# Kernel optimization log

Hardware: AMD Instinct MI355X
Metric: run time of the kernel (lower is better)

## Reference

```python
import jax, jax.numpy as jnp
import numpy as np
import math

D_MODEL = 1024
N_HEADS = 16
D_HEAD = D_MODEL // N_HEADS
B, S = 4, 2048


def setup_inputs() -> dict:
    key = jax.random.key(0)
    ks = jax.random.split(key, 9)
    std = 1.0 / math.sqrt(D_MODEL)
    x = jax.random.normal(ks[0], (B, S, D_MODEL), dtype=jnp.float32)
    # causal mask: True = masked out
    mask = jnp.triu(jnp.ones((S, S), dtype=bool), k=1)
    Wq = jax.random.normal(ks[1], (D_MODEL, D_MODEL), jnp.float32) * std
    bq = jnp.zeros((D_MODEL,), jnp.float32)
    Wk = jax.random.normal(ks[2], (D_MODEL, D_MODEL), jnp.float32) * std
    bk = jnp.zeros((D_MODEL,), jnp.float32)
    Wv = jax.random.normal(ks[3], (D_MODEL, D_MODEL), jnp.float32) * std
    bv = jnp.zeros((D_MODEL,), jnp.float32)
    Wo = jax.random.normal(ks[4], (D_MODEL, D_MODEL), jnp.float32) * std
    bo = jnp.zeros((D_MODEL,), jnp.float32)
    return {"x": x, "mask": mask, "Wq": Wq, "bq": bq, "Wk": Wk, "bk": bk,
            "Wv": Wv, "bv": bv, "Wo": Wo, "bo": bo}


def reference(x, mask, Wq, bq, Wk, bk, Wv, bv, Wo, bo):
    b, s, _ = x.shape
    scale = math.sqrt(D_HEAD)
    # projections (Linear: x @ W.T + b), reshape to [b, h, s, d]
    def proj(W, bias):
        y = jnp.einsum('bsd,ed->bse', x, W) + bias
        return y.reshape(b, s, N_HEADS, D_HEAD).transpose(0, 2, 1, 3)
    q = proj(Wq, bq)
    k = proj(Wk, bk)
    v = proj(Wv, bv)
    scores = jnp.einsum('bhqd,bhkd->bhqk', q, k) / scale  # [b,h,s,s]
    scores = jnp.where(mask[None, None, :, :], -jnp.inf, scores)
    attn = jax.nn.softmax(scores, axis=-1)
    # dropout is identity in eval mode
    out = jnp.einsum('bhqk,bhkd->bhqd', attn, v)
    out = out.transpose(0, 2, 1, 3).reshape(b, s, D_MODEL)
    return jnp.einsum('bsd,ed->bse', out, Wo) + bo
```

## Files before the change

kernel.cpp:

```cpp
#include <hip/hip_runtime.h>
#include <stdint.h>

#define NH 16
#define DH 64
#define DM 1024
#define Bz 4
#define Sz 2048

typedef __bf16 bf16x8 __attribute__((ext_vector_type(8)));
typedef float f32x4 __attribute__((ext_vector_type(4)));

#define GLD_LDS16(gsrc, ldst)                                             \
    __builtin_amdgcn_global_load_lds(                                     \
        (const __attribute__((address_space(1))) void*)(gsrc),            \
        (__attribute__((address_space(3))) void*)(ldst), 16, 0, 0)

__device__ __forceinline__ unsigned short f2bf(float f) {
    unsigned u = __float_as_uint(f);
    u += 0x7FFFu + ((u >> 16) & 1u);
    return (unsigned short)(u >> 16);
}
__device__ __forceinline__ float bf2f(unsigned short h) {
    return __uint_as_float(((unsigned)h) << 16);
}

__global__ void detect_dtype(const unsigned short* __restrict__ xs,
                             int* __restrict__ flagp)
{
    const int t = threadIdx.x;
    int cnt = 0;
    for (int i = 0; i < 64; i++) {
        const unsigned short h = xs[(t * 64 + i) * 2];
        const int e = (h >> 7) & 0xFF;
        if (h != 0 && e >= 100 && e <= 130) cnt++;
    }
#pragma unroll
    for (int off = 32; off >= 1; off >>= 1)
        cnt += __shfl_xor(cnt, off);
    if (t == 0) *flagp = (cnt < 2048) ? 1 : 0;
}

__global__ __launch_bounds__(256) void convert_inputs(
    const void* s0, const void* s1, const void* s2, const void* s3,
    const void* s4, const void* s5, const void* s6, const void* s7,
    const void* s8,
    unsigned short* d0, unsigned short* d1, unsigned short* d2,
    unsigned short* d3, unsigned short* d4, unsigned short* d5,
    unsigned short* d6, unsigned short* d7, unsigned short* d8,
    const int* __restrict__ flagp)
{
    const void* s; unsigned short* d; int n;
    switch (blockIdx.y) {
        case 0: s = s0; d = d0; n = Bz * Sz * DM; break;
        case 1: s = s1; d = d1; n = DM * DM; break;
        case 2: s = s2; d = d2; n = DM * DM; break;
        case 3: s = s3; d = d3; n = DM * DM; break;
        case 4: s = s4; d = d4; n = DM * DM; break;
        case 5: s = s5; d = d5; n = DM; break;
        case 6: s = s6; d = d6; n = DM; break;
        case 7: s = s7; d = d7; n = DM; break;
        default: s = s8; d = d8; n = DM; break;
    }
    const int flag   = *flagp;
    const int stride = gridDim.x * blockDim.x * 4;
    const int base   = (blockIdx.x * blockDim.x + threadIdx.x) * 4;
    if (flag) {
        const float* sf = (const float*)s;
        for (int i = base; i < n; i += stride) {
            const float4 v = *reinterpret_cast<const float4*>(&sf[i]);
            ushort2 a, b;
            a.x = f2bf(v.x); a.y = f2bf(v.y);
            b.x = f2bf(v.z); b.y = f2bf(v.w);
            *reinterpret_cast<ushort2*>(&d[i])     = a;
            *reinterpret_cast<ushort2*>(&d[i + 2]) = b;
        }
    } else {
        const unsigned short* sh = (const unsigned short*)s;
        for (int i = base; i < n; i += stride)
            *reinterpret_cast<uint2*>(&d[i]) = *reinterpret_cast<const uint2*>(&sh[i]);
    }
}

__global__ __launch_bounds__(256) void gemm_qkv(
    const unsigned short* __restrict__ X,
    const unsigned short* __restrict__ Wq,
    const unsigned short* __restrict__ Wk,
    const unsigned short* __restrict__ Wv,
    const unsigned short* __restrict__ bq,
    const unsigned short* __restrict__ bk,
    const unsigned short* __restrict__ bv,
    unsigned short* __restrict__ Qb,
    unsigned short* __restrict__ Kb,
    unsigned short* __restrict__ Vtb)
{
    __shared__ __align__(16) unsigned short As[4][128 * 32];
    __shared__ __align__(16) unsigned short Bs[4][128 * 32];
    const int tid  = threadIdx.x;
    const int w    = tid >> 6, lane = tid & 63;
    const int quad = lane >> 4, l15 = lane & 15;
    const int wm   = (w & 1) * 64, wn = (w >> 1) * 64;

    const int flat = (int)(blockIdx.y * gridDim.x + blockIdx.x);
    const int k8   = flat & 7;
    const int m    = flat >> 3;
    const int proj = m >> 6;
    const int mm   = m & 63;
    const int bm   = (k8 * 8 + (mm >> 3)) * 128;
    const int bn   = (mm & 7) * 128;

    const unsigned short* W      = proj == 0 ? Wq : (proj == 1 ? Wk : Wv);
    const unsigned short* bias_p = proj == 0 ? bq : (proj == 1 ? bk : bv);

    const int lrow = lane >> 2;
    const int lcol = (lane & 3) * 8;

    f32x4 acc[4][4];
    for (int i = 0; i < 4; i++)
        for (int j = 0; j < 4; j++)
            acc[i][j] = f32x4{0.f, 0.f, 0.f, 0.f};

    auto stage = [&](int buf, int ks) {
        const int k0 = ks << 5;
#pragma unroll
        for (int t = 0; t < 2; t++) {
            const int r = w * 32 + t * 16;
            GLD_LDS16(&X[(size_t)(bm + r + lrow) * DM + k0 + lcol], &As[buf][r * 32]);
            GLD_LDS16(&W[(size_t)(bn + r + lrow) * DM + k0 + lcol], &Bs[buf][r * 32]);
        }
    };

    auto compute32 = [&](int cur) {
        bf16x8 af[4], bfr[4];
#pragma unroll
        for (int i = 0; i < 4; i++)
            af[i] = *reinterpret_cast<const bf16x8*>(&As[cur][(wm + i * 16 + l15) * 32 + quad * 8]);
#pragma unroll
        for (int j = 0; j < 4; j++)
            bfr[j] = *reinterpret_cast<const bf16x8*>(&Bs[cur][(wn + j * 16 + l15) * 32 + quad * 8]);
#pragma unroll
        for (int i = 0; i < 4; i++)
#pragma unroll
            for (int j = 0; j < 4; j++)
                acc[i][j] = __builtin_amdgcn_mfma_f32_16x16x32_bf16(af[i], bfr[j], acc[i][j], 0, 0, 0);
    };

    stage(0, 0);
    stage(1, 1);
    for (int t = 0; t < 30; ++t) {
        stage((t + 2) & 3, t + 2);
        asm volatile("s_waitcnt vmcnt(8)" ::: "memory");
        __builtin_amdgcn_s_barrier();
        compute32(t & 3);
    }
    asm volatile("s_waitcnt vmcnt(4)" ::: "memory");
    __builtin_amdgcn_s_barrier();
    compute32(30 & 3);
    asm volatile("s_waitcnt vmcnt(0)" ::: "memory");
    __builtin_amdgcn_s_barrier();
    compute32(31 & 3);

    if (proj < 2) {
        unsigned short* dst = (proj == 0) ? Qb : Kb;
#pragma unroll
        for (int j = 0; j < 4; j++) {
            const int   e    = bn + wn + j * 16 + l15;
            const int   h    = e >> 6, dd = e & 63;
            const float bias = bf2f(bias_p[e]);
#pragma unroll
            for (int i = 0; i < 4; i++) {
#pragma unroll
                for (int r = 0; r < 4; r++) {
                    const int mrow = bm + wm + i * 16 + quad * 4 + r;
                    const int b = mrow >> 11, s = mrow & 2047;
                    dst[((size_t)(b * NH + h) * Sz + s) * DH + dd] = f2bf(acc[i][j][r] + bias);
                }
            }
        }
    } else {
#pragma unroll
        for (int j = 0; j < 4; j++) {
            const int   e    = bn + wn + j * 16 + l15;
            const int   h    = e >> 6, dd = e & 63;
            const float bias = bf2f(bias_p[e]);
#pragma unroll
            for (int i = 0; i < 4; i++) {
                const int m0 = bm + wm + i * 16 + quad * 4;
                const int b  = m0 >> 11, s0 = m0 & 2047;
                const unsigned u0 = __float_as_uint(acc[i][j][0] + bias) + 0x8000u;
                const unsigned u1 = __float_as_uint(acc[i][j][1] + bias) + 0x8000u;
                const unsigned u2 = __float_as_uint(acc[i][j][2] + bias) + 0x8000u;
                const unsigned u3 = __float_as_uint(acc[i][j][3] + bias) + 0x8000u;
                uint2 pk;
                pk.x = __builtin_amdgcn_perm(u1, u0, 0x07060302u);
                pk.y = __builtin_amdgcn_perm(u3, u2, 0x07060302u);
                *reinterpret_cast<uint2*>(
                    &Vtb[((size_t)(b * NH + h) * DH + dd) * Sz + s0]) = pk;
            }
        }
    }
}

__global__ __launch_bounds__(512) void flash_attn(
    const unsigned short* __restrict__ Qb,
    const unsigned short* __restrict__ Kb,
    const unsigned short* __restrict__ Vtb,
    unsigned short* __restrict__ AOb)
{
    __shared__ __align__(16) unsigned short Ks[64 * 72];
    __shared__ __align__(16) unsigned short Vs[64 * 72];
    __shared__ __align__(16) unsigned short Ps[128 * 72];

    const int tid  = threadIdx.x;
    const int w    = tid >> 6, lane = tid & 63;
    const int quad = lane >> 4, l15 = lane & 15;

    const int flat = (int)(blockIdx.y * gridDim.x + blockIdx.x);
    const int k8   = flat & 7;
    const int m    = flat >> 3;
    const int bh   = k8 + 8 * (m >> 3);
    const int cA   = m & 7;

    const int srow = tid >> 3;
    const int scc  = (tid & 7) * 8;
    const int hh = bh & 15, bb = bh >> 4;

    for (int pass = 0; pass < 2; pass++) {
        const int chunk = pass ? (15 - cA) : cA;
        const int qb = chunk * 128;
        const int qw = qb + w * 16;

        const size_t qbase = ((size_t)bh * Sz + qw + l15) * DH;
        const bf16x8 qf0 = *reinterpret_cast<const bf16x8*>(&Qb[qbase + quad * 8]);
        const bf16x8 qf1 = *reinterpret_cast<const bf16x8*>(&Qb[qbase + 32 + quad * 8]);

        f32x4 o[4];
#pragma unroll
        for (int jd = 0; jd < 4; jd++) o[jd] = f32x4{0.f, 0.f, 0.f, 0.f};
        float lsum = 0.f;

        const int n_kv = qb + 128;

        auto compute = [&](int kb) {
            const bool need_mask = (kb + 64 > qw);
#pragma unroll
            for (int j = 0; j < 4; j++) {
                const bf16x8 kf0 = *reinterpret_cast<const bf16x8*>(&Ks[(j * 16 + l15) * 72 + quad * 8]);
                const bf16x8 kf1 = *reinterpret_cast<const bf16x8*>(&Ks[(j * 16 + l15) * 72 + 32 + quad * 8]);
                f32x4 st = f32x4{0.f, 0.f, 0.f, 0.f};
                st = __builtin_amdgcn_mfma_f32_16x16x32_bf16(kf0, qf0, st, 0, 0, 0);
                st = __builtin_amdgcn_mfma_f32_16x16x32_bf16(kf1, qf1, st, 0, 0, 0);
                const int qa = qw + l15;
                float p[4];
#pragma unroll
                for (int r = 0; r < 4; r++) {
                    float e = __builtin_amdgcn_exp2f(st[r] * 0.18033688011f);
                    if (need_mask) {
                        const int kv = kb + j * 16 + quad * 4 + r;
                        e = (kv <= qa) ? e : 0.f;
                    }
                    p[r] = e;
                }
                lsum += (p[0] + p[1]) + (p[2] + p[3]);
                const unsigned u0 = __float_as_uint(p[0]) + 0x8000u;
                const unsigned u1 = __float_as_uint(p[1]) + 0x8000u;
                const unsigned u2 = __float_as_uint(p[2]) + 0x8000u;
                const unsigned u3 = __float_as_uint(p[3]) + 0x8000u;
                const unsigned pk0 = __builtin_amdgcn_perm(u1, u0, 0x07060302u);
                const unsigned pk1 = __builtin_amdgcn_perm(u3, u2, 0x07060302u);
                const int prow = (w * 16 + l15) * 72 + j * 16 + quad * 4;
                *reinterpret_cast<unsigned*>(&Ps[prow])     = pk0;
                *reinterpret_cast<unsigned*>(&Ps[prow + 2]) = pk1;
            }

            asm volatile("s_waitcnt lgkmcnt(0)" ::: "memory");

            const bf16x8 pf0 = *reinterpret_cast<const bf16x8*>(&Ps[(w * 16 + l15) * 72 + quad * 8]);
            const bf16x8 pf1 = *reinterpret_cast<const bf16x8*>(&Ps[(w * 16 + l15) * 72 + 32 + quad * 8]);
#pragma unroll
            for (int jd = 0; jd < 4; jd++) {
                const bf16x8 vf0 = *reinterpret_cast<const bf16x8*>(&Vs[(jd * 16 + l15) * 72 + quad * 8]);
                const bf16x8 vf1 = *reinterpret_cast<const bf16x8*>(&Vs[(jd * 16 + l15) * 72 + 32 + quad * 8]);
                o[jd] = __builtin_amdgcn_mfma_f32_16x16x32_bf16(pf0, vf0, o[jd], 0, 0, 0);
                o[jd] = __builtin_amdgcn_mfma_f32_16x16x32_bf16(pf1, vf1, o[jd], 0, 0, 0);
            }
        };

        uint4 kr0 = *reinterpret_cast<const uint4*>(&Kb[((size_t)bh * Sz + srow) * DH + scc]);
        uint4 vr0 = *reinterpret_cast<const uint4*>(&Vtb[((size_t)bh * DH + srow) * Sz + scc]);
        uint4 kr1, vr1;

        for (int kb = 0; kb < n_kv; kb += 128) {
            __syncthreads();
            *reinterpret_cast<uint4*>(&Ks[srow * 72 + scc]) = kr0;
            *reinterpret_cast<uint4*>(&Vs[srow * 72 + scc]) = vr0;
            kr1 = *reinterpret_cast<const uint4*>(&Kb[((size_t)bh * Sz + kb + 64 + srow) * DH + scc]);
            vr1 = *reinterpret_cast<const uint4*>(&Vtb[((size_t)bh * DH + srow) * Sz + kb + 64 + scc]);
            asm volatile("s_waitcnt lgkmcnt(0)" ::: "memory");
            __builtin_amdgcn_s_barrier();
            asm volatile("" ::: "memory");
            if (kb <= qw + 15) compute(kb);

            __syncthreads();
            *reinterpret_cast<uint4*>(&Ks[srow * 72 + scc]) = kr1;
            *reinterpret_cast<uint4*>(&Vs[srow * 72 + scc]) = vr1;
            if (kb + 128 < n_kv) {
                kr0 = *reinterpret_cast<const uint4*>(&Kb[((size_t)bh * Sz + kb + 128 + srow) * DH + scc]);
                vr0 = *reinterpret_cast<const uint4*>(&Vtb[((size_t)bh * DH + srow) * Sz + kb + 128 + scc]);
            }
            asm volatile("s_waitcnt lgkmcnt(0)" ::: "memory");
            __builtin_amdgcn_s_barrier();
            asm volatile("" ::: "memory");
            if (kb + 64 <= qw + 15) compute(kb + 64);
        }

        lsum += __shfl_xor(lsum, 16);
        lsum += __shfl_xor(lsum, 32);

        float linv[4];
#pragma unroll
        for (int r = 0; r < 4; r++)
            linv[r] = 1.0f / __shfl(lsum, quad * 4 + r);
#pragma unroll
        for (int jd = 0; jd < 4; jd++) {
#pragma unroll
            for (int r = 0; r < 4; r++) {
                const int s = qw + quad * 4 + r;
                AOb[((size_t)(bb * Sz + s)) * DM + hh * DH + jd * 16 + l15] =
                    f2bf(o[jd][r] * linv[r]);
            }
        }
    }
}

__global__ __launch_bounds__(256) void gemm_out(
    const unsigned short* __restrict__ A,
    const unsigned short* __restrict__ W,
    const unsigned short* __restrict__ bo,
    void* __restrict__ outv,
    const int* __restrict__ flagp)
{
    __shared__ __align__(16) unsigned short As[4][128 * 32];
    __shared__ __align__(16) unsigned short Bs[4][128 * 32];
    const int tid  = threadIdx.x;
    const int w    = tid >> 6, lane = tid & 63;
    const int quad = lane >> 4, l15 = lane & 15;
    const int wm   = (w & 1) * 64, wn = (w >> 1) * 64;

    const int flat = (int)(blockIdx.y * gridDim.x + blockIdx.x);
    const int k8   = flat & 7;
    const int m    = flat >> 3;
    const int bm   = (k8 * 8 + (m >> 3)) * 128;
    const int bn   = (m & 7) * 128;

    const int lrow = lane >> 2;
    const int lcol = (lane & 3) * 8;

    f32x4 acc[4][4];
    for (int i = 0; i < 4; i++)
        for (int j = 0; j < 4; j++)
            acc[i][j] = f32x4{0.f, 0.f, 0.f, 0.f};

    auto stage = [&](int buf, int ks) {
        const int k0 = ks << 5;
#pragma unroll
        for (int t = 0; t < 2; t++) {
            const int r = w * 32 + t * 16;
            GLD_LDS16(&A[(size_t)(bm + r + lrow) * DM + k0 + lcol], &As[buf][r * 32]);
            GLD_LDS16(&W[(size_t)(bn + r + lrow) * DM + k0 + lcol], &Bs[buf][r * 32]);
        }
    };

    auto compute32 = [&](int cur) {
        bf16x8 af[4], bfr[4];
#pragma unroll
        for (int i = 0; i < 4; i++)
            af[i] = *reinterpret_cast<const bf16x8*>(&As[cur][(wm + i * 16 + l15) * 32 + quad * 8]);
#pragma unroll
        for (int j = 0; j < 4; j++)
            bfr[j] = *reinterpret_cast<const bf16x8*>(&Bs[cur][(wn + j * 16 + l15) * 32 + quad * 8]);
#pragma unroll
        for (int i = 0; i < 4; i++)
#pragma unroll
            for (int j = 0; j < 4; j++)
                acc[i][j] = __builtin_amdgcn_mfma_f32_16x16x32_bf16(af[i], bfr[j], acc[i][j], 0, 0, 0);
    };

    stage(0, 0);
    stage(1, 1);
    for (int t = 0; t < 30; ++t) {
        stage((t + 2) & 3, t + 2);
        asm volatile("s_waitcnt vmcnt(8)" ::: "memory");
        __builtin_amdgcn_s_barrier();
        compute32(t & 3);
    }
    asm volatile("s_waitcnt vmcnt(4)" ::: "memory");
    __builtin_amdgcn_s_barrier();
    compute32(30 & 3);
    asm volatile("s_waitcnt vmcnt(0)" ::: "memory");
    __builtin_amdgcn_s_barrier();
    compute32(31 & 3);

    const int flag = *flagp;
    float*          outf = (float*)outv;
    unsigned short* outh = (unsigned short*)outv;
#pragma unroll
    for (int j = 0; j < 4; j++) {
        const int   e    = bn + wn + j * 16 + l15;
        const float bias = bf2f(bo[e]);
#pragma unroll
        for (int i = 0; i < 4; i++) {
#pragma unroll
            for (int r = 0; r < 4; r++) {
                const int   mrow = bm + wm + i * 16 + quad * 4 + r;
                const float v = acc[i][j][r] + bias;
                if (flag) outf[(size_t)mrow * DM + e] = v;
                else      outh[(size_t)mrow * DM + e] = f2bf(v);
            }
        }
    }
}

extern "C" void kernel_launch(void* const* d_in, const int* in_sizes, int n_in,
                              void* d_out, int out_size, void* d_ws, size_t ws_size,
                              hipStream_t stream) {
    const void* x = nullptr;
    const void* Wsrc[4] = {nullptr, nullptr, nullptr, nullptr};
    const void* bsrc[4] = {nullptr, nullptr, nullptr, nullptr};
    int nw = 0, nb = 0;
    for (int i = 0; i < n_in; i++) {
        const int sz = in_sizes[i];
        if (sz == Bz * Sz * DM)            { if (!x) x = d_in[i]; }
        else if (sz == DM * DM)            { if (nw < 4) Wsrc[nw++] = d_in[i]; }
        else if (sz == DM)                 { if (nb < 4) bsrc[nb++] = d_in[i]; }
    }

    char* wsb = (char*)d_ws;
    int*  flagp = (int*)wsb;
    unsigned short* Xc  = (unsigned short*)(wsb + 16);
    const size_t NX = (size_t)Bz * Sz * DM;
    const size_t NW = (size_t)DM * DM;
    unsigned short* Wc0 = Xc  + NX;
    unsigned short* Wc1 = Wc0 + NW;
    unsigned short* Wc2 = Wc1 + NW;
    unsigned short* Wc3 = Wc2 + NW;
    unsigned short* bc0 = Wc3 + NW;
    unsigned short* bc1 = bc0 + DM;
    unsigned short* bc2 = bc1 + DM;
    unsigned short* bc3 = bc2 + DM;
    unsigned short* Qb  = bc3 + DM;
    const size_t SZ = (size_t)Bz * NH * Sz * DH;
    unsigned short* Kb  = Qb  + SZ;
    unsigned short* Vtb = Kb  + SZ;
    unsigned short* AOb = Vtb + SZ;

    detect_dtype<<<1, 64, 0, stream>>>((const unsigned short*)x, flagp);
    convert_inputs<<<dim3(512, 9), 256, 0, stream>>>(
        x, Wsrc[0], Wsrc[1], Wsrc[2], Wsrc[3],
        bsrc[0], bsrc[1], bsrc[2], bsrc[3],
        Xc, Wc0, Wc1, Wc2, Wc3, bc0, bc1, bc2, bc3, flagp);

    gemm_qkv <<<dim3(24, 64), 256, 0, stream>>>(Xc, Wc0, Wc1, Wc2, bc0, bc1, bc2, Qb, Kb, Vtb);
    flash_attn<<<dim3(8, 64), 512, 0, stream>>>(Qb, Kb, Vtb, AOb);
    gemm_out <<<dim3(8, 64), 256, 0, stream>>>(AOb, Wc3, bc3, d_out, flagp);
}
```

Before: 303.6 us.

## Retile QKV and output GEMMs to 256x256 blocks with swizzled LDS

Both projection GEMMs move from 128x128 tiles with a 4-stage K=32 pipeline to 256x256 tiles using 512 threads, K=64 double-buffered LDS staging, and an XOR-swizzled LDS layout. MFMA groups are wrapped in s_setprio. The intent is more data reuse per block, fewer LDS bank conflicts, and better overlap of math with global loads. The cost is a large LDS footprint of 128KB per block, which limits how many blocks fit per CU. Grids also shrink to 384 and 128 blocks, so the output GEMM may leave many CUs idle and the work may be spread unevenly.

Result: slower. 316.4 us (+4.2%).

```diff
diff --git a/kernel.cpp b/kernel.cpp
--- a/kernel.cpp
+++ b/kernel.cpp
@@ -6,6 +6,7 @@
 #define DM 1024
 #define Bz 4
 #define Sz 2048
+#define NKT 16
 
 typedef __bf16 bf16x8 __attribute__((ext_vector_type(8)));
 typedef float f32x4 __attribute__((ext_vector_type(4)));
@@ -81,7 +82,14 @@
     }
 }
 
-__global__ __launch_bounds__(256) void gemm_qkv(
+
+__device__ __forceinline__ bf16x8 lds_frag(const unsigned short* lds, int R, int c) {
+    const int cs = c ^ ((R & 7) << 4);
+    return *reinterpret_cast<const bf16x8*>(
+        reinterpret_cast<const char*>(lds) + R * 128 + cs);
+}
+
+__global__ __launch_bounds__(512, 2) void gemm_qkv(
     const unsigned short* __restrict__ X,
     const unsigned short* __restrict__ Wq,
     const unsigned short* __restrict__ Wk,
@@ -93,103 +101,157 @@
     unsigned short* __restrict__ Kb,
     unsigned short* __restrict__ Vtb)
 {
-    __shared__ __align__(16) unsigned short As[4][128 * 32];
-    __shared__ __align__(16) unsigned short Bs[4][128 * 32];
+    __shared__ __align__(16) unsigned short Alds[2][256 * 64];
+    __shared__ __align__(16) unsigned short Blds[2][256 * 64];
+
     const int tid  = threadIdx.x;
     const int w    = tid >> 6, lane = tid & 63;
     const int quad = lane >> 4, l15 = lane & 15;
-    const int wm   = (w & 1) * 64, wn = (w >> 1) * 64;
-
-    const int flat = (int)(blockIdx.y * gridDim.x + blockIdx.x);
+    const int wr   = w >> 2, wc = w & 3;
+
+    const int flat = (int)blockIdx.x;
     const int k8   = flat & 7;
     const int m    = flat >> 3;
-    const int proj = m >> 6;
-    const int mm   = m & 63;
-    const int bm   = (k8 * 8 + (mm >> 3)) * 128;
-    const int bn   = (mm & 7) * 128;
+    const int proj = m >> 4;
+    const int mm   = m & 15;
+    const int bm   = (k8 * 4 + (mm >> 2)) * 256;
+    const int bn   = (mm & 3) * 256;
 
     const unsigned short* W      = proj == 0 ? Wq : (proj == 1 ? Wk : Wv);
     const unsigned short* bias_p = proj == 0 ? bq : (proj == 1 ? bk : bv);
-
-    const int lrow = lane >> 2;
-    const int lcol = (lane & 3) * 8;
-
-    f32x4 acc[4][4];
-    for (int i = 0; i < 4; i++)
+    const unsigned short* Abase  = X + (size_t)bm * DM;
+    const unsigned short* Bbase  = W + (size_t)bn * DM;
+
+    const int srow = 8 * w + (lane >> 3);
+    const int scb  = (lane & 7) * 16;
+    const int ssc  = scb ^ ((srow & 7) << 4);
+
+    f32x4 acc[8][4];
+#pragma unroll
+    for (int i = 0; i < 8; i++)
+#pragma unroll
         for (int j = 0; j < 4; j++)
             acc[i][j] = f32x4{0.f, 0.f, 0.f, 0.f};
 
-    auto stage = [&](int buf, int ks) {
-        const int k0 = ks << 5;
-#pragma unroll
-        for (int t = 0; t < 2; t++) {
-            const int r = w * 32 + t * 16;
-            GLD_LDS16(&X[(size_t)(bm + r + lrow) * DM + k0 + lcol], &As[buf][r * 32]);
-            GLD_LDS16(&W[(size_t)(bn + r + lrow) * DM + k0 + lcol], &Bs[buf][r * 32]);
+    auto stage_tile = [&](int buf, int kt) {
+        const int kc = kt * 64;
+#pragma unroll
+        for (int q = 0; q < 2; q++) {
+            const int r  = srow + 64 * q;
+            const int ld = (64 * q + 8 * w) * 64;
+            GLD_LDS16(&Abase[(size_t)(r      ) * DM + kc + (ssc >> 1)], &Alds[buf][ld]);
+            GLD_LDS16(&Abase[(size_t)(r + 128) * DM + kc + (ssc >> 1)], &Alds[buf][ld + 128 * 64]);
+            GLD_LDS16(&Bbase[(size_t)(r      ) * DM + kc + (ssc >> 1)], &Blds[buf][ld]);
+            GLD_LDS16(&Bbase[(size_t)(r + 128) * DM + kc + (ssc >> 1)], &Blds[buf][ld + 128 * 64]);
         }
     };
 
-    auto compute32 = [&](int cur) {
-        bf16x8 af[4], bfr[4];
-#pragma unroll
-        for (int i = 0; i < 4; i++)
-            af[i] = *reinterpret_cast<const bf16x8*>(&As[cur][(wm + i * 16 + l15) * 32 + quad * 8]);
-#pragma unroll
-        for (int j = 0; j < 4; j++)
-            bfr[j] = *reinterpret_cast<const bf16x8*>(&Bs[cur][(wn + j * 16 + l15) * 32 + quad * 8]);
-#pragma unroll
-        for (int i = 0; i < 4; i++)
-#pragma unroll
-            for (int j = 0; j < 4; j++)
-                acc[i][j] = __builtin_amdgcn_mfma_f32_16x16x32_bf16(af[i], bfr[j], acc[i][j], 0, 0, 0);
-    };
-
-    stage(0, 0);
-    stage(1, 1);
-    for (int t = 0; t < 30; ++t) {
-        stage((t + 2) & 3, t + 2);
-        asm volatile("s_waitcnt vmcnt(8)" ::: "memory");
-        __builtin_amdgcn_s_barrier();
-        compute32(t & 3);
-    }
-    asm volatile("s_waitcnt vmcnt(4)" ::: "memory");
-    __builtin_amdgcn_s_barrier();
-    compute32(30 & 3);
+    stage_tile(0, 0);
     asm volatile("s_waitcnt vmcnt(0)" ::: "memory");
     __builtin_amdgcn_s_barrier();
-    compute32(31 & 3);
+    asm volatile("" ::: "memory");
+
+    for (int T = 0; T < NKT; ++T) {
+        const int cur = T & 1;
+        if (T < NKT - 1) stage_tile(cur ^ 1, T + 1);
+
+        const unsigned short* A = &Alds[cur][0];
+        const unsigned short* B = &Blds[cur][0];
+        const int aR0 = wr * 128 + l15;
+        const int bR0 = wc * 64 + l15;
+
+        bf16x8 aR[4][2], b01[2][2], b23[2][2];
+#pragma unroll
+        for (int mi = 0; mi < 4; mi++) {
+            aR[mi][0] = lds_frag(A, aR0 + mi * 16, quad * 16);
+            aR[mi][1] = lds_frag(A, aR0 + mi * 16, quad * 16 + 64);
+        }
+#pragma unroll
+        for (int nj = 0; nj < 2; nj++) {
+            b01[nj][0] = lds_frag(B, bR0 + nj * 16, quad * 16);
+            b01[nj][1] = lds_frag(B, bR0 + nj * 16, quad * 16 + 64);
+        }
+        __builtin_amdgcn_s_setprio(1);
+#pragma unroll
+        for (int mi = 0; mi < 4; mi++)
+#pragma unroll
+            for (int nj = 0; nj < 2; nj++) {
+                acc[mi][nj] = __builtin_amdgcn_mfma_f32_16x16x32_bf16(aR[mi][0], b01[nj][0], acc[mi][nj], 0, 0, 0);
+                acc[mi][nj] = __builtin_amdgcn_mfma_f32_16x16x32_bf16(aR[mi][1], b01[nj][1], acc[mi][nj], 0, 0, 0);
+            }
+        __builtin_amdgcn_s_setprio(0);
+#pragma unroll
+        for (int nj = 0; nj < 2; nj++) {
+            b23[nj][0] = lds_frag(B, bR0 + (nj + 2) * 16, quad * 16);
+            b23[nj][1] = lds_frag(B, bR0 + (nj + 2) * 16, quad * 16 + 64);
+        }
+        __builtin_amdgcn_s_setprio(1);
+#pragma unroll
+        for (int mi = 0; mi < 4; mi++)
+#pragma unroll
+            for (int nj = 0; nj < 2; nj++) {
+                acc[mi][nj + 2] = __builtin_amdgcn_mfma_f32_16x16x32_bf16(aR[mi][0], b23[nj][0], acc[mi][nj + 2], 0, 0, 0);
+                acc[mi][nj + 2] = __builtin_amdgcn_mfma_f32_16x16x32_bf16(aR[mi][1], b23[nj][1], acc[mi][nj + 2], 0, 0, 0);
+            }
+        __builtin_amdgcn_s_setprio(0);
+#pragma unroll
+        for (int mi = 0; mi < 4; mi++) {
+            aR[mi][0] = lds_frag(A, aR0 + (mi + 4) * 16, quad * 16);
+            aR[mi][1] = lds_frag(A, aR0 + (mi + 4) * 16, quad * 16 + 64);
+        }
+        __builtin_amdgcn_s_setprio(1);
+#pragma unroll
+        for (int mi = 0; mi < 4; mi++)
+#pragma unroll
+            for (int nj = 0; nj < 2; nj++) {
+                acc[mi + 4][nj + 2] = __builtin_amdgcn_mfma_f32_16x16x32_bf16(aR[mi][0], b23[nj][0], acc[mi + 4][nj + 2], 0, 0, 0);
+                acc[mi + 4][nj + 2] = __builtin_amdgcn_mfma_f32_16x16x32_bf16(aR[mi][1], b23[nj][1], acc[mi + 4][nj + 2], 0, 0, 0);
+            }
+#pragma unroll
+        for (int mi = 0; mi < 4; mi++)
+#pragma unroll
+            for (int nj = 0; nj < 2; nj++) {
+                acc[mi + 4][nj] = __builtin_amdgcn_mfma_f32_16x16x32_bf16(aR[mi][0], b01[nj][0], acc[mi + 4][nj], 0, 0, 0);
+                acc[mi + 4][nj] = __builtin_amdgcn_mfma_f32_16x16x32_bf16(aR[mi][1], b01[nj][1], acc[mi + 4][nj], 0, 0, 0);
+            }
+        __builtin_amdgcn_s_setprio(0);
+
+        asm volatile("s_waitcnt vmcnt(0)" ::: "memory");
+        __builtin_amdgcn_s_barrier();
+        asm volatile("" ::: "memory");
+    }
 
     if (proj < 2) {
         unsigned short* dst = (proj == 0) ? Qb : Kb;
 #pragma unroll
-        for (int j = 0; j < 4; j++) {
-            const int   e    = bn + wn + j * 16 + l15;
+        for (int nj = 0; nj < 4; nj++) {
+            const int   e    = bn + wc * 64 + nj * 16 + l15;
             const int   h    = e >> 6, dd = e & 63;
             const float bias = bf2f(bias_p[e]);
 #pragma unroll
-            for (int i = 0; i < 4; i++) {
+            for (int mi = 0; mi < 8; mi++) {
 #pragma unroll
                 for (int r = 0; r < 4; r++) {
-                    const int mrow = bm + wm + i * 16 + quad * 4 + r;
+                    const int mrow = bm + wr * 128 + mi * 16 + quad * 4 + r;
                     const int b = mrow >> 11, s = mrow & 2047;
-                    dst[((size_t)(b * NH + h) * Sz + s) * DH + dd] = f2bf(acc[i][j][r] + bias);
+                    dst[((size_t)(b * NH + h) * Sz + s) * DH + dd] = f2bf(acc[mi][nj][r] + bias);
                 }
             }
         }
     } else {
 #pragma unroll
-        for (int j = 0; j < 4; j++) {
-            const int   e    = bn + wn + j * 16 + l15;
+        for (int nj = 0; nj < 4; nj++) {
+            const int   e    = bn + wc * 64 + nj * 16 + l15;
             const int   h    = e >> 6, dd = e & 63;
             const float bias = bf2f(bias_p[e]);
 #pragma unroll
-            for (int i = 0; i < 4; i++) {
-                const int m0 = bm + wm + i * 16 + quad * 4;
+            for (int mi = 0; mi < 8; mi++) {
+                const int m0 = bm + wr * 128 + mi * 16 + quad * 4;
                 const int b  = m0 >> 11, s0 = m0 & 2047;
-                const unsigned u0 = __float_as_uint(acc[i][j][0] + bias) + 0x8000u;
-                const unsigned u1 = __float_as_uint(acc[i][j][1] + bias) + 0x8000u;
-                const unsigned u2 = __float_as_uint(acc[i][j][2] + bias) + 0x8000u;
-                const unsigned u3 = __float_as_uint(acc[i][j][3] + bias) + 0x8000u;
+                const unsigned u0 = __float_as_uint(acc[mi][nj][0] + bias) + 0x8000u;
+                const unsigned u1 = __float_as_uint(acc[mi][nj][1] + bias) + 0x8000u;
+                const unsigned u2 = __float_as_uint(acc[mi][nj][2] + bias) + 0x8000u;
+                const unsigned u3 = __float_as_uint(acc[mi][nj][3] + bias) + 0x8000u;
                 uint2 pk;
                 pk.x = __builtin_amdgcn_perm(u1, u0, 0x07060302u);
                 pk.y = __builtin_amdgcn_perm(u3, u2, 0x07060302u);
@@ -332,87 +394,142 @@
     }
 }
 
-__global__ __launch_bounds__(256) void gemm_out(
-    const unsigned short* __restrict__ A,
+__global__ __launch_bounds__(512, 2) void gemm_out(
+    const unsigned short* __restrict__ Ain,
     const unsigned short* __restrict__ W,
     const unsigned short* __restrict__ bo,
     void* __restrict__ outv,
     const int* __restrict__ flagp)
 {
-    __shared__ __align__(16) unsigned short As[4][128 * 32];
-    __shared__ __align__(16) unsigned short Bs[4][128 * 32];
+    __shared__ __align__(16) unsigned short Alds[2][256 * 64];
+    __shared__ __align__(16) unsigned short Blds[2][256 * 64];
+
     const int tid  = threadIdx.x;
     const int w    = tid >> 6, lane = tid & 63;
     const int quad = lane >> 4, l15 = lane & 15;
-    const int wm   = (w & 1) * 64, wn = (w >> 1) * 64;
-
-    const int flat = (int)(blockIdx.y * gridDim.x + blockIdx.x);
+    const int wr   = w >> 2, wc = w & 3;
+
+    const int flat = (int)blockIdx.x;
     const int k8   = flat & 7;
     const int m    = flat >> 3;
-    const int bm   = (k8 * 8 + (m >> 3)) * 128;
-    const int bn   = (m & 7) * 128;
-
-    const int lrow = lane >> 2;
-    const int lcol = (lane & 3) * 8;
-
-    f32x4 acc[4][4];
-    for (int i = 0; i < 4; i++)
+    const int bm   = (k8 * 4 + (m >> 2)) * 256;
+    const int bn   = (m & 3) * 256;
+
+    const unsigned short* Abase = Ain + (size_t)bm * DM;
+    const unsigned short* Bbase = W   + (size_t)bn * DM;
+
+    const int srow = 8 * w + (lane >> 3);
+    const int scb  = (lane & 7) * 16;
+    const int ssc  = scb ^ ((srow & 7) << 4);
+
+    f32x4 acc[8][4];
+#pragma unroll
+    for (int i = 0; i < 8; i++)
+#pragma unroll
         for (int j = 0; j < 4; j++)
             acc[i][j] = f32x4{0.f, 0.f, 0.f, 0.f};
 
-    auto stage = [&](int buf, int ks) {
-        const int k0 = ks << 5;
-#pragma unroll
-        for (int t = 0; t < 2; t++) {
-            const int r = w * 32 + t * 16;
-            GLD_LDS16(&A[(size_t)(bm + r + lrow) * DM + k0 + lcol], &As[buf][r * 32]);
-            GLD_LDS16(&W[(size_t)(bn + r + lrow) * DM + k0 + lcol], &Bs[buf][r * 32]);
+    auto stage_tile = [&](int buf, int kt) {
+        const int kc = kt * 64;
+#pragma unroll
+        for (int q = 0; q < 2; q++) {
+            const int r  = srow + 64 * q;
+            const int ld = (64 * q + 8 * w) * 64;
+            GLD_LDS16(&Abase[(size_t)(r      ) * DM + kc + (ssc >> 1)], &Alds[buf][ld]);
+            GLD_LDS16(&Abase[(size_t)(r + 128) * DM + kc + (ssc >> 1)], &Alds[buf][ld + 128 * 64]);
+            GLD_LDS16(&Bbase[(size_t)(r      ) * DM + kc + (ssc >> 1)], &Blds[buf][ld]);
+            GLD_LDS16(&Bbase[(size_t)(r + 128) * DM + kc + (ssc >> 1)], &Blds[buf][ld + 128 * 64]);
         }
     };
 
-    auto compute32 = [&](int cur) {
-        bf16x8 af[4], bfr[4];
-#pragma unroll
-        for (int i = 0; i < 4; i++)
-            af[i] = *reinterpret_cast<const bf16x8*>(&As[cur][(wm + i * 16 + l15) * 32 + quad * 8]);
-#pragma unroll
-        for (int j = 0; j < 4; j++)
-            bfr[j] = *reinterpret_cast<const bf16x8*>(&Bs[cur][(wn + j * 16 + l15) * 32 + quad * 8]);
-#pragma unroll
-        for (int i = 0; i < 4; i++)
-#pragma unroll
-            for (int j = 0; j < 4; j++)
-                acc[i][j] = __builtin_amdgcn_mfma_f32_16x16x32_bf16(af[i], bfr[j], acc[i][j], 0, 0, 0);
-    };
-
-    stage(0, 0);
-    stage(1, 1);
-    for (int t = 0; t < 30; ++t) {
-        stage((t + 2) & 3, t + 2);
-        asm volatile("s_waitcnt vmcnt(8)" ::: "memory");
-        __builtin_amdgcn_s_barrier();
-        compute32(t & 3);
-    }
-    asm volatile("s_waitcnt vmcnt(4)" ::: "memory");
-    __builtin_amdgcn_s_barrier();
-    compute32(30 & 3);
+    stage_tile(0, 0);
     asm volatile("s_waitcnt vmcnt(0)" ::: "memory");
     __builtin_amdgcn_s_barrier();
-    compute32(31 & 3);
+    asm volatile("" ::: "memory");
+
+    for (int T = 0; T < NKT; ++T) {
+        const int cur = T & 1;
+        if (T < NKT - 1) stage_tile(cur ^ 1, T + 1);
+
+        const unsigned short* A = &Alds[cur][0];
+        const unsigned short* B = &Blds[cur][0];
+        const int aR0 = wr * 128 + l15;
+        const int bR0 = wc * 64 + l15;
+
+        bf16x8 aR[4][2], b01[2][2], b23[2][2];
+#pragma unroll
+        for (int mi = 0; mi < 4; mi++) {
+            aR[mi][0] = lds_frag(A, aR0 + mi * 16, quad * 16);
+            aR[mi][1] = lds_frag(A, aR0 + mi * 16, quad * 16 + 64);
+        }
+#pragma unroll
+        for (int nj = 0; nj < 2; nj++) {
+            b01[nj][0] = lds_frag(B, bR0 + nj * 16, quad * 16);
+            b01[nj][1] = lds_frag(B, bR0 + nj * 16, quad * 16 + 64);
+        }
+        __builtin_amdgcn_s_setprio(1);
+#pragma unroll
+        for (int mi = 0; mi < 4; mi++)
+#pragma unroll
+            for (int nj = 0; nj < 2; nj++) {
+                acc[mi][nj] = __builtin_amdgcn_mfma_f32_16x16x32_bf16(aR[mi][0], b01[nj][0], acc[mi][nj], 0, 0, 0);
+                acc[mi][nj] = __builtin_amdgcn_mfma_f32_16x16x32_bf16(aR[mi][1], b01[nj][1], acc[mi][nj], 0, 0, 0);
+            }
+        __builtin_amdgcn_s_setprio(0);
+#pragma unroll
+        for (int nj = 0; nj < 2; nj++) {
+            b23[nj][0] = lds_frag(B, bR0 + (nj + 2) * 16, quad * 16);
+            b23[nj][1] = lds_frag(B, bR0 + (nj + 2) * 16, quad * 16 + 64);
+        }
+        __builtin_amdgcn_s_setprio(1);
+#pragma unroll
+        for (int mi = 0; mi < 4; mi++)
+#pragma unroll
+            for (int nj = 0; nj < 2; nj++) {
+                acc[mi][nj + 2] = __builtin_amdgcn_mfma_f32_16x16x32_bf16(aR[mi][0], b23[nj][0], acc[mi][nj + 2], 0, 0, 0);
+                acc[mi][nj + 2] = __builtin_amdgcn_mfma_f32_16x16x32_bf16(aR[mi][1], b23[nj][1], acc[mi][nj + 2], 0, 0, 0);
+            }
+        __builtin_amdgcn_s_setprio(0);
+#pragma unroll
+        for (int mi = 0; mi < 4; mi++) {
+            aR[mi][0] = lds_frag(A, aR0 + (mi + 4) * 16, quad * 16);
+            aR[mi][1] = lds_frag(A, aR0 + (mi + 4) * 16, quad * 16 + 64);
+        }
+        __builtin_amdgcn_s_setprio(1);
+#pragma unroll
+        for (int mi = 0; mi < 4; mi++)
+#pragma unroll
+            for (int nj = 0; nj < 2; nj++) {
+                acc[mi + 4][nj + 2] = __builtin_amdgcn_mfma_f32_16x16x32_bf16(aR[mi][0], b23[nj][0], acc[mi + 4][nj + 2], 0, 0, 0);
+                acc[mi + 4][nj + 2] = __builtin_amdgcn_mfma_f32_16x16x32_bf16(aR[mi][1], b23[nj][1], acc[mi + 4][nj + 2], 0, 0, 0);
+            }
+#pragma unroll
+        for (int mi = 0; mi < 4; mi++)
+#pragma unroll
+            for (int nj = 0; nj < 2; nj++) {
+                acc[mi + 4][nj] = __builtin_amdgcn_mfma_f32_16x16x32_bf16(aR[mi][0], b01[nj][0], acc[mi + 4][nj], 0, 0, 0);
+                acc[mi + 4][nj] = __builtin_amdgcn_mfma_f32_16x16x32_bf16(aR[mi][1], b01[nj][1], acc[mi + 4][nj], 0, 0, 0);
+            }
+        __builtin_amdgcn_s_setprio(0);
+
+        asm volatile("s_waitcnt vmcnt(0)" ::: "memory");
+        __builtin_amdgcn_s_barrier();
+        asm volatile("" ::: "memory");
+    }
 
     const int flag = *flagp;
     float*          outf = (float*)outv;
     unsigned short* outh = (unsigned short*)outv;
 #pragma unroll
-    for (int j = 0; j < 4; j++) {
-        const int   e    = bn + wn + j * 16 + l15;
+    for (int nj = 0; nj < 4; nj++) {
+        const int   e    = bn + wc * 64 + nj * 16 + l15;
         const float bias = bf2f(bo[e]);
 #pragma unroll
-        for (int i = 0; i < 4; i++) {
+        for (int mi = 0; mi < 8; mi++) {
 #pragma unroll
             for (int r = 0; r < 4; r++) {
-                const int   mrow = bm + wm + i * 16 + quad * 4 + r;
-                const float v = acc[i][j][r] + bias;
+                const int   mrow = bm + wr * 128 + mi * 16 + quad * 4 + r;
+                const float v = acc[mi][nj][r] + bias;
                 if (flag) outf[(size_t)mrow * DM + e] = v;
                 else      outh[(size_t)mrow * DM + e] = f2bf(v);
             }
@@ -459,7 +576,7 @@
         bsrc[0], bsrc[1], bsrc[2], bsrc[3],
         Xc, Wc0, Wc1, Wc2, Wc3, bc0, bc1, bc2, bc3, flagp);
 
-    gemm_qkv <<<dim3(24, 64), 256, 0, stream>>>(Xc, Wc0, Wc1, Wc2, bc0, bc1, bc2, Qb, Kb, Vtb);
+    gemm_qkv <<<dim3(384), 512, 0, stream>>>(Xc, Wc0, Wc1, Wc2, bc0, bc1, bc2, Qb, Kb, Vtb);
     flash_attn<<<dim3(8, 64), 512, 0, stream>>>(Qb, Kb, Vtb, AOb);
-    gemm_out <<<dim3(8, 64), 256, 0, stream>>>(AOb, Wc3, bc3, d_out, flagp);
-}
+    gemm_out <<<dim3(128), 512, 0, stream>>>(AOb, Wc3, bc3, d_out, flagp);
+}
```

## Use 32x32x16 MFMA with XOR-swizzled K=64 LDS tiles in projection GEMMs

Applied to the files above, without the earlier changes.

Both projection GEMMs switch from 16x16x32 MFMA tiles to 32x32x16 MFMA with 2x2 accumulators per wave. LDS staging moves from a 4-deep K=32 ring to double-buffered K=64 tiles with an XOR swizzle, to cut LDS bank conflicts and halve the number of barriers. The launch bounds now request 2 blocks per SM. The cost is a full vmcnt(0) wait every iteration, so prefetch overlap is shallower.

Result: faster. 288.3 us (-5.0%).

```diff
diff --git a/kernel.cpp b/kernel.cpp
--- a/kernel.cpp
+++ b/kernel.cpp
@@ -6,9 +6,11 @@
 #define DM 1024
 #define Bz 4
 #define Sz 2048
+#define NKT 16
 
 typedef __bf16 bf16x8 __attribute__((ext_vector_type(8)));
 typedef float f32x4 __attribute__((ext_vector_type(4)));
+typedef float f32x16 __attribute__((ext_vector_type(16)));
 
 #define GLD_LDS16(gsrc, ldst)                                             \
     __builtin_amdgcn_global_load_lds(                                     \
@@ -81,7 +83,8 @@
     }
 }
 
-__global__ __launch_bounds__(256) void gemm_qkv(
+
+__global__ __launch_bounds__(256, 2) void gemm_qkv(
     const unsigned short* __restrict__ X,
     const unsigned short* __restrict__ Wq,
     const unsigned short* __restrict__ Wk,
@@ -93,11 +96,12 @@
     unsigned short* __restrict__ Kb,
     unsigned short* __restrict__ Vtb)
 {
-    __shared__ __align__(16) unsigned short As[4][128 * 32];
-    __shared__ __align__(16) unsigned short Bs[4][128 * 32];
+    __shared__ __align__(16) unsigned short As[2][128 * 64];
+    __shared__ __align__(16) unsigned short Bs[2][128 * 64];
+
     const int tid  = threadIdx.x;
     const int w    = tid >> 6, lane = tid & 63;
-    const int quad = lane >> 4, l15 = lane & 15;
+    const int l31  = lane & 31, half = lane >> 5;
     const int wm   = (w & 1) * 64, wn = (w >> 1) * 64;
 
     const int flat = (int)(blockIdx.y * gridDim.x + blockIdx.x);
@@ -110,91 +114,102 @@
 
     const unsigned short* W      = proj == 0 ? Wq : (proj == 1 ? Wk : Wv);
     const unsigned short* bias_p = proj == 0 ? bq : (proj == 1 ? bk : bv);
-
-    const int lrow = lane >> 2;
-    const int lcol = (lane & 3) * 8;
-
-    f32x4 acc[4][4];
-    for (int i = 0; i < 4; i++)
-        for (int j = 0; j < 4; j++)
-            acc[i][j] = f32x4{0.f, 0.f, 0.f, 0.f};
-
-    auto stage = [&](int buf, int ks) {
-        const int k0 = ks << 5;
-#pragma unroll
-        for (int t = 0; t < 2; t++) {
-            const int r = w * 32 + t * 16;
-            GLD_LDS16(&X[(size_t)(bm + r + lrow) * DM + k0 + lcol], &As[buf][r * 32]);
-            GLD_LDS16(&W[(size_t)(bn + r + lrow) * DM + k0 + lcol], &Bs[buf][r * 32]);
+    const unsigned short* Abase  = X + (size_t)bm * DM;
+    const unsigned short* Bbase  = W + (size_t)bn * DM;
+
+    const int sr8 = lane >> 3;
+    const int sce = ((lane & 7) ^ sr8) * 8;
+
+    f32x16 acc[2][2];
+#pragma unroll
+    for (int i = 0; i < 2; i++)
+#pragma unroll
+        for (int j = 0; j < 2; j++)
+#pragma unroll
+            for (int e = 0; e < 16; e++)
+                acc[i][j][e] = 0.f;
+
+    auto stage = [&](int buf, int kt) {
+        const int kc = kt * 64;
+#pragma unroll
+        for (int t = 0; t < 4; t++) {
+            const int r = w * 32 + t * 8;
+            GLD_LDS16(&Abase[(size_t)(r + sr8) * DM + kc + sce], &As[buf][r * 64]);
+            GLD_LDS16(&Bbase[(size_t)(r + sr8) * DM + kc + sce], &Bs[buf][r * 64]);
         }
     };
 
-    auto compute32 = [&](int cur) {
-        bf16x8 af[4], bfr[4];
-#pragma unroll
-        for (int i = 0; i < 4; i++)
-            af[i] = *reinterpret_cast<const bf16x8*>(&As[cur][(wm + i * 16 + l15) * 32 + quad * 8]);
-#pragma unroll
-        for (int j = 0; j < 4; j++)
-            bfr[j] = *reinterpret_cast<const bf16x8*>(&Bs[cur][(wn + j * 16 + l15) * 32 + quad * 8]);
-#pragma unroll
-        for (int i = 0; i < 4; i++)
-#pragma unroll
-            for (int j = 0; j < 4; j++)
-                acc[i][j] = __builtin_amdgcn_mfma_f32_16x16x32_bf16(af[i], bfr[j], acc[i][j], 0, 0, 0);
+    auto frg = [&](const unsigned short* base, int row, int cb) {
+        const int cs = cb ^ ((row & 7) << 4);
+        return *reinterpret_cast<const bf16x8*>(
+            reinterpret_cast<const char*>(base) + row * 128 + cs);
     };
 
     stage(0, 0);
-    stage(1, 1);
-    for (int t = 0; t < 30; ++t) {
-        stage((t + 2) & 3, t + 2);
-        asm volatile("s_waitcnt vmcnt(8)" ::: "memory");
-        __builtin_amdgcn_s_barrier();
-        compute32(t & 3);
-    }
-    asm volatile("s_waitcnt vmcnt(4)" ::: "memory");
-    __builtin_amdgcn_s_barrier();
-    compute32(30 & 3);
     asm volatile("s_waitcnt vmcnt(0)" ::: "memory");
     __builtin_amdgcn_s_barrier();
-    compute32(31 & 3);
+    asm volatile("" ::: "memory");
+
+    for (int T = 0; T < NKT; ++T) {
+        if (T < NKT - 1) stage((T + 1) & 1, T + 1);
+        const unsigned short* A = &As[T & 1][0];
+        const unsigned short* B = &Bs[T & 1][0];
+#pragma unroll
+        for (int s = 0; s < 4; s++) {
+            const int cb = s * 32 + half * 16;
+            const bf16x8 a0 = frg(A, wm + l31,      cb);
+            const bf16x8 a1 = frg(A, wm + 32 + l31, cb);
+            const bf16x8 b0 = frg(B, wn + l31,      cb);
+            const bf16x8 b1 = frg(B, wn + 32 + l31, cb);
+            acc[0][0] = __builtin_amdgcn_mfma_f32_32x32x16_bf16(a0, b0, acc[0][0], 0, 0, 0);
+            acc[0][1] = __builtin_amdgcn_mfma_f32_32x32x16_bf16(a0, b1, acc[0][1], 0, 0, 0);
+            acc[1][0] = __builtin_amdgcn_mfma_f32_32x32x16_bf16(a1, b0, acc[1][0], 0, 0, 0);
+            acc[1][1] = __builtin_amdgcn_mfma_f32_32x32x16_bf16(a1, b1, acc[1][1], 0, 0, 0);
+        }
+        asm volatile("s_waitcnt vmcnt(0)" ::: "memory");
+        __builtin_amdgcn_s_barrier();
+        asm volatile("" ::: "memory");
+    }
 
     if (proj < 2) {
         unsigned short* dst = (proj == 0) ? Qb : Kb;
 #pragma unroll
-        for (int j = 0; j < 4; j++) {
-            const int   e    = bn + wn + j * 16 + l15;
+        for (int nj = 0; nj < 2; nj++) {
+            const int   e    = bn + wn + nj * 32 + l31;
             const int   h    = e >> 6, dd = e & 63;
             const float bias = bf2f(bias_p[e]);
 #pragma unroll
-            for (int i = 0; i < 4; i++) {
-#pragma unroll
-                for (int r = 0; r < 4; r++) {
-                    const int mrow = bm + wm + i * 16 + quad * 4 + r;
+            for (int mi = 0; mi < 2; mi++) {
+#pragma unroll
+                for (int reg = 0; reg < 16; reg++) {
+                    const int mrow = bm + wm + mi * 32 + (reg & 3) + 8 * (reg >> 2) + 4 * half;
                     const int b = mrow >> 11, s = mrow & 2047;
-                    dst[((size_t)(b * NH + h) * Sz + s) * DH + dd] = f2bf(acc[i][j][r] + bias);
+                    dst[((size_t)(b * NH + h) * Sz + s) * DH + dd] = f2bf(acc[mi][nj][reg] + bias);
                 }
             }
         }
     } else {
 #pragma unroll
-        for (int j = 0; j < 4; j++) {
-            const int   e    = bn + wn + j * 16 + l15;
+        for (int nj = 0; nj < 2; nj++) {
+            const int   e    = bn + wn + nj * 32 + l31;
             const int   h    = e >> 6, dd = e & 63;
             const float bias = bf2f(bias_p[e]);
 #pragma unroll
-            for (int i = 0; i < 4; i++) {
-                const int m0 = bm + wm + i * 16 + quad * 4;
-                const int b  = m0 >> 11, s0 = m0 & 2047;
-                const unsigned u0 = __float_as_uint(acc[i][j][0] + bias) + 0x8000u;
-                const unsigned u1 = __float_as_uint(acc[i][j][1] + bias) + 0x8000u;
-                const unsigned u2 = __float_as_uint(acc[i][j][2] + bias) + 0x8000u;
-                const unsigned u3 = __float_as_uint(acc[i][j][3] + bias) + 0x8000u;
-                uint2 pk;
-                pk.x = __builtin_amdgcn_perm(u1, u0, 0x07060302u);
-                pk.y = __builtin_amdgcn_perm(u3, u2, 0x07060302u);
-                *reinterpret_cast<uint2*>(
-                    &Vtb[((size_t)(b * NH + h) * DH + dd) * Sz + s0]) = pk;
+            for (int mi = 0; mi < 2; mi++) {
+#pragma unroll
+                for (int g = 0; g < 4; g++) {
+                    const int m0 = bm + wm + mi * 32 + 8 * g + 4 * half;
+                    const int b  = m0 >> 11, s0 = m0 & 2047;
+                    const unsigned u0 = __float_as_uint(acc[mi][nj][4 * g + 0] + bias) + 0x8000u;
+                    const unsigned u1 = __float_as_uint(acc[mi][nj][4 * g + 1] + bias) + 0x8000u;
+                    const unsigned u2 = __float_as_uint(acc[mi][nj][4 * g + 2] + bias) + 0x8000u;
+                    const unsigned u3 = __float_as_uint(acc[mi][nj][4 * g + 3] + bias) + 0x8000u;
+                    uint2 pk;
+                    pk.x = __builtin_amdgcn_perm(u1, u0, 0x07060302u);
+                    pk.y = __builtin_amdgcn_perm(u3, u2, 0x07060302u);
+                    *reinterpret_cast<uint2*>(
+                        &Vtb[((size_t)(b * NH + h) * DH + dd) * Sz + s0]) = pk;
+                }
             }
         }
     }
@@ -332,18 +347,19 @@
     }
 }
 
-__global__ __launch_bounds__(256) void gemm_out(
-    const unsigned short* __restrict__ A,
+__global__ __launch_bounds__(256, 2) void gemm_out(
+    const unsigned short* __restrict__ Ain,
     const unsigned short* __restrict__ W,
     const unsigned short* __restrict__ bo,
     void* __restrict__ outv,
     const int* __restrict__ flagp)
 {
-    __shared__ __align__(16) unsigned short As[4][128 * 32];
-    __shared__ __align__(16) unsigned short Bs[4][128 * 32];
+    __shared__ __align__(16) unsigned short As[2][128 * 64];
+    __shared__ __align__(16) unsigned short Bs[2][128 * 64];
+
     const int tid  = threadIdx.x;
     const int w    = tid >> 6, lane = tid & 63;
-    const int quad = lane >> 4, l15 = lane & 15;
+    const int l31  = lane & 31, half = lane >> 5;
     const int wm   = (w & 1) * 64, wn = (w >> 1) * 64;
 
     const int flat = (int)(blockIdx.y * gridDim.x + blockIdx.x);
@@ -352,67 +368,76 @@
     const int bm   = (k8 * 8 + (m >> 3)) * 128;
     const int bn   = (m & 7) * 128;
 
-    const int lrow = lane >> 2;
-    const int lcol = (lane & 3) * 8;
-
-    f32x4 acc[4][4];
-    for (int i = 0; i < 4; i++)
-        for (int j = 0; j < 4; j++)
-            acc[i][j] = f32x4{0.f, 0.f, 0.f, 0.f};
-
-    auto stage = [&](int buf, int ks) {
-        const int k0 = ks << 5;
-#pragma unroll
-        for (int t = 0; t < 2; t++) {
-            const int r = w * 32 + t * 16;
-            GLD_LDS16(&A[(size_t)(bm + r + lrow) * DM + k0 + lcol], &As[buf][r * 32]);
-            GLD_LDS16(&W[(size_t)(bn + r + lrow) * DM + k0 + lcol], &Bs[buf][r * 32]);
+    const unsigned short* Abase = Ain + (size_t)bm * DM;
+    const unsigned short* Bbase = W   + (size_t)bn * DM;
+
+    const int sr8 = lane >> 3;
+    const int sce = ((lane & 7) ^ sr8) * 8;
+
+    f32x16 acc[2][2];
+#pragma unroll
+    for (int i = 0; i < 2; i++)
+#pragma unroll
+        for (int j = 0; j < 2; j++)
+#pragma unroll
+            for (int e = 0; e < 16; e++)
+                acc[i][j][e] = 0.f;
+
+    auto stage = [&](int buf, int kt) {
+        const int kc = kt * 64;
+#pragma unroll
+        for (int t = 0; t < 4; t++) {
+            const int r = w * 32 + t * 8;
+            GLD_LDS16(&Abase[(size_t)(r + sr8) * DM + kc + sce], &As[buf][r * 64]);
+            GLD_LDS16(&Bbase[(size_t)(r + sr8) * DM + kc + sce], &Bs[buf][r * 64]);
         }
     };
 
-    auto compute32 = [&](int cur) {
-        bf16x8 af[4], bfr[4];
-#pragma unroll
-        for (int i = 0; i < 4; i++)
-            af[i] = *reinterpret_cast<const bf16x8*>(&As[cur][(wm + i * 16 + l15) * 32 + quad * 8]);
-#pragma unroll
-        for (int j = 0; j < 4; j++)
-            bfr[j] = *reinterpret_cast<const bf16x8*>(&Bs[cur][(wn + j * 16 + l15) * 32 + quad * 8]);
-#pragma unroll
-        for (int i = 0; i < 4; i++)
-#pragma unroll
-            for (int j = 0; j < 4; j++)
-                acc[i][j] = __builtin_amdgcn_mfma_f32_16x16x32_bf16(af[i], bfr[j], acc[i][j], 0, 0, 0);
+    auto frg = [&](const unsigned short* base, int row, int cb) {
+        const int cs = cb ^ ((row & 7) << 4);
+        return *reinterpret_cast<const bf16x8*>(
+            reinterpret_cast<const char*>(base) + row * 128 + cs);
     };
 
     stage(0, 0);
-    stage(1, 1);
-    for (int t = 0; t < 30; ++t) {
-        stage((t + 2) & 3, t + 2);
-        asm volatile("s_waitcnt vmcnt(8)" ::: "memory");
-        __builtin_amdgcn_s_barrier();
-        compute32(t & 3);
-    }
-    asm volatile("s_waitcnt vmcnt(4)" ::: "memory");
-    __builtin_amdgcn_s_barrier();
-    compute32(30 & 3);
     asm volatile("s_waitcnt vmcnt(0)" ::: "memory");
     __builtin_amdgcn_s_barrier();
-    compute32(31 & 3);
+    asm volatile("" ::: "memory");
+
+    for (int T = 0; T < NKT; ++T) {
+        if (T < NKT - 1) stage((T + 1) & 1, T + 1);
+        const unsigned short* A = &As[T & 1][0];
+        const unsigned short* B = &Bs[T & 1][0];
+#pragma unroll
+        for (int s = 0; s < 4; s++) {
+            const int cb = s * 32 + half * 16;
+            const bf16x8 a0 = frg(A, wm + l31,      cb);
+            const bf16x8 a1 = frg(A, wm + 32 + l31, cb);
+            const bf16x8 b0 = frg(B, wn + l31,      cb);
+            const bf16x8 b1 = frg(B, wn + 32 + l31, cb);
+            acc[0][0] = __builtin_amdgcn_mfma_f32_32x32x16_bf16(a0, b0, acc[0][0], 0, 0, 0);
+            acc[0][1] = __builtin_amdgcn_mfma_f32_32x32x16_bf16(a0, b1, acc[0][1], 0, 0, 0);
+            acc[1][0] = __builtin_amdgcn_mfma_f32_32x32x16_bf16(a1, b0, acc[1][0], 0, 0, 0);
+            acc[1][1] = __builtin_amdgcn_mfma_f32_32x32x16_bf16(a1, b1, acc[1][1], 0, 0, 0);
+        }
+        asm volatile("s_waitcnt vmcnt(0)" ::: "memory");
+        __builtin_amdgcn_s_barrier();
+        asm volatile("" ::: "memory");
+    }
 
     const int flag = *flagp;
     float*          outf = (float*)outv;
     unsigned short* outh = (unsigned short*)outv;
 #pragma unroll
-    for (int j = 0; j < 4; j++) {
-        const int   e    = bn + wn + j * 16 + l15;
+    for (int nj = 0; nj < 2; nj++) {
+        const int   e    = bn + wn + nj * 32 + l31;
         const float bias = bf2f(bo[e]);
 #pragma unroll
-        for (int i = 0; i < 4; i++) {
-#pragma unroll
-            for (int r = 0; r < 4; r++) {
-                const int   mrow = bm + wm + i * 16 + quad * 4 + r;
-                const float v = acc[i][j][r] + bias;
+        for (int mi = 0; mi < 2; mi++) {
+#pragma unroll
+            for (int reg = 0; reg < 16; reg++) {
+                const int   mrow = bm + wm + mi * 32 + (reg & 3) + 8 * (reg >> 2) + 4 * half;
+                const float v = acc[mi][nj][reg] + bias;
                 if (flag) outf[(size_t)mrow * DM + e] = v;
                 else      outh[(size_t)mrow * DM + e] = f2bf(v);
             }
```
